# Optimization experiments

Measured on AMD Instinct MI355X. Metric: run time of the kernel, lower is better.

Reference implementation:

```python
import jax, jax.numpy as jnp
import numpy as np

H, DH, M, DIN = 8, 64, 32, 512  # heads, head_dim, cluster_num, input_dim
INNER = H * DH


def setup_inputs() -> dict:
    key = jax.random.key(0)
    ks = jax.random.split(key, 12)
    s = 0.02
    B, N = 4, 16384
    return {
        "x": jax.random.normal(ks[0], (B, N, DIN), jnp.float32),
        "Wx": jax.random.normal(ks[1], (INNER, DIN), jnp.float32) * s,
        "bx": jnp.zeros((INNER,), jnp.float32),
        "Wfx": jax.random.normal(ks[2], (INNER, DIN), jnp.float32) * s,
        "bfx": jnp.zeros((INNER,), jnp.float32),
        "Wslice": jax.random.normal(ks[3], (M, DH), jnp.float32) * s,
        "bslice": jnp.zeros((M,), jnp.float32),
        "Wq": jax.random.normal(ks[4], (DH, DH), jnp.float32) * s,
        "Wk": jax.random.normal(ks[5], (DH, DH), jnp.float32) * s,
        "Wv": jax.random.normal(ks[6], (DH, DH), jnp.float32) * s,
        "Wout": jax.random.normal(ks[7], (DIN, INNER), jnp.float32) * s,
        "bout": jnp.zeros((DIN,), jnp.float32),
        "temperature": jnp.full((1, H, 1, 1), 0.5, jnp.float32),
    }


def reference(x, Wx, bx, Wfx, bfx, Wslice, bslice, Wq, Wk, Wv, Wout, bout, temperature):
    B, N, D = x.shape
    scale = DH ** -0.5
    # projections -> [B, H, N, DH]
    x_mid = (x @ Wx.T + bx).reshape(B, N, H, DH).transpose(0, 2, 1, 3)
    fx_mid = (x @ Wfx.T + bfx).reshape(B, N, H, DH).transpose(0, 2, 1, 3)
    # soft clustering: [B, H, N, M]
    slice_logits = (x_mid @ Wslice.T + bslice) / temperature
    slice_weights = jax.nn.softmax(slice_logits, axis=-1)
    slice_norm = slice_weights.sum(axis=2)  # [B, H, M]
    slice_token = jnp.einsum('bhnd,bhnm->bhmd', fx_mid, slice_weights)
    slice_token = slice_token / (slice_norm[:, :, :, None] + 1e-5)
    # tiny cluster-level attention (M=32)
    q = slice_token @ Wq.T
    k = slice_token @ Wk.T
    v = slice_token @ Wv.T
    attn = jax.nn.softmax(jnp.einsum('bhmd,bhkd->bhmk', q, k) * scale, axis=-1)
    out_slice = jnp.einsum('bhmk,bhkd->bhmd', attn, v)
    # de-slice back to tokens: [B, H, N, DH] -> [B, N, H*DH]
    out_x = jnp.einsum('bhmd,bhnm->bhnd', out_slice, slice_weights)
    out_x = out_x.transpose(0, 2, 1, 3).reshape(B, N, INNER)
    return out_x @ Wout.T + bout
```

## Files before the change

### kernel.cpp

```cpp
#include <hip/hip_runtime.h>

#define B_ 4
#define N_ 16384
#define DIN_ 512
#define H_ 8
#define DH_ 64
#define M_ 32
#define HM_ 256
#define INNER_ 512
#define K2_PARTS 16
#define K2_NIT 32

typedef _Float16 fp16_t;
typedef _Float16 h8 __attribute__((ext_vector_type(8)));
typedef _Float16 h4 __attribute__((ext_vector_type(4)));
typedef float f4 __attribute__((ext_vector_type(4)));


__device__ __forceinline__ int swz(int n, int hm) {
  return ((((hm >> 3) ^ ((n >> 3) & 3)) << 3) | (hm & 7));
}

__global__ __launch_bounds__(256) void k0_prep(
    const float* __restrict__ Wx, const float* __restrict__ bx,
    const float* __restrict__ Wslice, const float* __restrict__ bslice,
    const float* __restrict__ temperature,
    fp16_t* __restrict__ Wcb, float* __restrict__ bcomp) {
  __shared__ float ws[M_ * DH_];
  const int h = blockIdx.x;
  const int tid = threadIdx.x;
  for (int i = tid; i < M_ * DH_; i += 256) ws[i] = Wslice[i];
  __syncthreads();
  const float invt = 1.0f / temperature[h];
  for (int m = 0; m < M_; ++m) {
    const int hm = h * M_ + m;
    for (int k = tid; k < DIN_; k += 256) {
      float acc = 0.f;
      #pragma unroll 16
      for (int d = 0; d < DH_; ++d)
        acc += ws[m * DH_ + d] * Wx[(size_t)(h * DH_ + d) * DIN_ + k];
      const int tile = (k >> 5) * 16 + (hm >> 4);
      const int ln = (((k >> 3) & 3) << 4) + (hm & 15);
      Wcb[(size_t)tile * 512 + ln * 8 + (k & 7)] = (fp16_t)(acc * invt);
    }
  }
  if (tid < M_) {
    const int m = tid;
    float acc = bslice[m];
    for (int d = 0; d < DH_; ++d) acc += ws[m * DH_ + d] * bx[h * DH_ + d];
    bcomp[h * M_ + m] = acc * invt;
  }
}

__global__ __launch_bounds__(256) void k1_logits(
    const float* __restrict__ x, const fp16_t* __restrict__ Wcb,
    const float* __restrict__ bcomp, fp16_t* __restrict__ w_blk,
    fp16_t* __restrict__ wt_blk, fp16_t* __restrict__ xt_blk) {
  __shared__ __align__(16) fp16_t smem[16896];
  fp16_t* lt = smem;
  const int tid = threadIdx.x;
  const int lane = tid & 63;
  const int wv = tid >> 6;
  const int n0 = blockIdx.x * 64;
  const int b = blockIdx.y;
  f4 acc[4][4] = {};
  const float* xb = x + ((size_t)b * N_ + n0) * DIN_;
  const int lrow = lane & 15;
  const int kb = (lane >> 4) * 8;
  const int xr = tid >> 3, xq = tid & 7;
  const int xt_rt = wv >> 1;
  const int xt_nt = wv & 1;
  const int xt_k = xt_rt * 16 + (lane & 15);
  const int xt_nb = xt_nt * 32 + (lane >> 4) * 8;
  const fp16_t* wp = Wcb + (size_t)(wv * 4) * 512 + lane * 8;

  f4 xv[2];
  h8 bfv[4];
  #pragma unroll
  for (int i = 0; i < 2; ++i)
    xv[i] = *(const f4*)(xb + (size_t)(xr + i * 32) * DIN_ + xq * 4);
  #pragma unroll
  for (int t = 0; t < 4; ++t)
    bfv[t] = *(const h8*)(wp + (size_t)t * 512);
  #pragma unroll
  for (int i = 0; i < 2; ++i) {
    h4 hv = {(fp16_t)xv[i].x, (fp16_t)xv[i].y, (fp16_t)xv[i].z, (fp16_t)xv[i].w};
    *(h4*)&smem[(xr + i * 32) * 40 + xq * 4] = hv;
  }
  __syncthreads();

  for (int kt = 0; kt < 16; ++kt) {
    fp16_t* lxc = smem + (kt & 1) * 2560;
    fp16_t* lxn = smem + ((kt & 1) ^ 1) * 2560;
    h8 bf[4];
    #pragma unroll
    for (int t = 0; t < 4; ++t) bf[t] = bfv[t];
    if (kt < 15) {
      const int k0n = (kt + 1) * 32;
      #pragma unroll
      for (int i = 0; i < 2; ++i)
        xv[i] = *(const f4*)(xb + (size_t)(xr + i * 32) * DIN_ + k0n + xq * 4);
      #pragma unroll
      for (int t = 0; t < 4; ++t)
        bfv[t] = *(const h8*)(wp + (size_t)((kt + 1) * 16 + t) * 512);
    }
    {
      h8 tx;
      #pragma unroll
      for (int e = 0; e < 8; ++e) tx[e] = lxc[(xt_nb + e) * 40 + xt_k];
      *(h8*)(xt_blk + (((size_t)(b * 32 + kt * 2 + xt_rt) * (N_ / 32)) + (n0 >> 5) + xt_nt) * 512 + lane * 8) = tx;
    }
    h8 af[4];
    #pragma unroll
    for (int t = 0; t < 4; ++t) af[t] = *(const h8*)&lxc[(t * 16 + lrow) * 40 + kb];
    #pragma unroll
    for (int tn = 0; tn < 4; ++tn)
      #pragma unroll
      for (int tc = 0; tc < 4; ++tc)
        acc[tn][tc] = __builtin_amdgcn_mfma_f32_16x16x32_f16(af[tn], bf[tc], acc[tn][tc], 0, 0, 0);
    if (kt < 15) {
      #pragma unroll
      for (int i = 0; i < 2; ++i) {
        h4 hv = {(fp16_t)xv[i].x, (fp16_t)xv[i].y, (fp16_t)xv[i].z, (fp16_t)xv[i].w};
        *(h4*)&lxn[(xr + i * 32) * 40 + xq * 4] = hv;
      }
    }
    __syncthreads();
  }

  const int col = lane & 15;
  const int rgrp = (lane >> 4) * 4;
  float bc[2][2];
  #pragma unroll
  for (int s = 0; s < 2; ++s) {
    bc[s][0] = bcomp[wv * 64 + s * 32 + col];
    bc[s][1] = bcomp[wv * 64 + s * 32 + 16 + col];
  }
  #pragma unroll
  for (int s = 0; s < 2; ++s) {
    const int hmA = wv * 64 + s * 32 + col;
    #pragma unroll
    for (int tn = 0; tn < 4; ++tn)
      #pragma unroll
      for (int r = 0; r < 4; ++r) {
        const int nl = tn * 16 + rgrp + r;
        lt[nl * 264 + swz(nl, hmA)] = (fp16_t)(acc[tn][2 * s][r] + bc[s][0]);
        lt[nl * 264 + swz(nl, hmA + 16)] = (fp16_t)(acc[tn][2 * s + 1][r] + bc[s][1]);
      }
  }
  __syncthreads();

  #pragma unroll
  for (int p = 0; p < 2; ++p) {
    const int pair = tid + p * 256;
    const int nl = pair >> 3, h = pair & 7;
    const int sw = (nl >> 3) & 3;
    h8 ch[4];
    #pragma unroll
    for (int q = 0; q < 4; ++q)
      ch[q] = *(const h8*)&lt[nl * 264 + ((h * 4 + q) ^ sw) * 8];
    float v[32];
    #pragma unroll
    for (int q = 0; q < 4; ++q)
      #pragma unroll
      for (int e = 0; e < 8; ++e) v[q * 8 + e] = (float)ch[q][e];
    float mx = v[0];
    #pragma unroll
    for (int j = 1; j < 32; ++j) mx = fmaxf(mx, v[j]);
    float sm = 0.f;
    #pragma unroll
    for (int j = 0; j < 32; ++j) { v[j] = __expf(v[j] - mx); sm += v[j]; }
    const float inv = __builtin_amdgcn_rcpf(sm);
    h8 oc[4];
    #pragma unroll
    for (int q = 0; q < 4; ++q)
      #pragma unroll
      for (int e = 0; e < 8; ++e) oc[q][e] = (fp16_t)(v[q * 8 + e] * inv);
    #pragma unroll
    for (int q = 0; q < 4; ++q)
      *(h8*)&lt[nl * 264 + ((h * 4 + q) ^ sw) * 8] = oc[q];
  }
  __syncthreads();

  #pragma unroll
  for (int p = 0; p < 8; ++p) {
    const int tile = p * 4 + wv;
    const int nt_l = tile >> 3, hmb = tile & 7;
    const int n_l = nt_l * 16 + (lane & 15);
    const int g = hmb * 4 + (lane >> 4);
    const int sw = (n_l >> 3) & 3;
    h8 v = *(const h8*)&lt[n_l * 264 + (g ^ sw) * 8];
    *(h8*)(w_blk + (((size_t)(b * (N_ / 16) + (n0 >> 4) + nt_l)) * 8 + hmb) * 512 + lane * 8) = v;
  }

  #pragma unroll
  for (int p = 0; p < 8; ++p) {
    const int tile = p * 4 + wv;
    const int hmt = tile >> 1, ntl = tile & 1;
    const int hm = hmt * 16 + (lane & 15);
    const int nb = ntl * 32 + (lane >> 4) * 8;
    h8 v;
    #pragma unroll
    for (int e = 0; e < 8; ++e) {
      const int n = nb + e;
      v[e] = lt[n * 264 + swz(n, hm)];
    }
    *(h8*)(wt_blk + (((size_t)(b * 16 + hmt)) * (N_ / 32) + (n0 >> 5) + ntl) * 512 + lane * 8) = v;
  }
}

__global__ __launch_bounds__(256) void k2_S(
    const fp16_t* __restrict__ wt_blk, const fp16_t* __restrict__ xt_blk,
    float* __restrict__ P, float* __restrict__ norm) {
  const int tid = threadIdx.x, lane = tid & 63, wv = tid >> 6;
  const int hm0 = (blockIdx.x & 1) * 128;
  const int kc0 = (blockIdx.x >> 1) * 128;
  const int part = blockIdx.y;
  const int nt0 = part * K2_NIT;
  const int b = blockIdx.z;
  const int hmw = (wv & 1) * 64, kw = (wv >> 1) * 64;
  const int hmt0 = (hm0 + hmw) >> 4;
  const int kt0 = (kc0 + kw) >> 4;
  const fp16_t* ap = wt_blk + (((size_t)(b * 16 + hmt0)) * (N_ / 32) + nt0) * 512 + lane * 8;
  const fp16_t* bp = xt_blk + (((size_t)(b * 32 + kt0)) * (N_ / 32) + nt0) * 512 + lane * 8;
  const size_t arow = (size_t)(N_ / 32) * 512;
  f4 acc[4][4] = {};
  float ns[4] = {0.f, 0.f, 0.f, 0.f};
  const bool do_norm = (kc0 == 0) && (kw == 0);

  h8 aA[4], bA[4], aB[4], bB[4];
  #pragma unroll
  for (int t = 0; t < 4; ++t) {
    aA[t] = *(const h8*)(ap + (size_t)t * arow);
    bA[t] = *(const h8*)(bp + (size_t)t * arow);
  }
  for (int it = 0; it < K2_NIT; it += 2) {
    #pragma unroll
    for (int t = 0; t < 4; ++t) {
      aB[t] = *(const h8*)(ap + (size_t)t * arow + (it + 1) * 512);
      bB[t] = *(const h8*)(bp + (size_t)t * arow + (it + 1) * 512);
    }
    #pragma unroll
    for (int tn = 0; tn < 4; ++tn)
      #pragma unroll
      for (int tc = 0; tc < 4; ++tc)
        acc[tn][tc] = __builtin_amdgcn_mfma_f32_16x16x32_f16(aA[tn], bA[tc], acc[tn][tc], 0, 0, 0);
    if (do_norm) {
      #pragma unroll
      for (int t = 0; t < 4; ++t)
        #pragma unroll
        for (int e = 0; e < 8; ++e) ns[t] += (float)aA[t][e];
    }
    if (it + 2 < K2_NIT) {
      #pragma unroll
      for (int t = 0; t < 4; ++t) {
        aA[t] = *(const h8*)(ap + (size_t)t * arow + (it + 2) * 512);
        bA[t] = *(const h8*)(bp + (size_t)t * arow + (it + 2) * 512);
      }
    }
    #pragma unroll
    for (int tn = 0; tn < 4; ++tn)
      #pragma unroll
      for (int tc = 0; tc < 4; ++tc)
        acc[tn][tc] = __builtin_amdgcn_mfma_f32_16x16x32_f16(aB[tn], bB[tc], acc[tn][tc], 0, 0, 0);
    if (do_norm) {
      #pragma unroll
      for (int t = 0; t < 4; ++t)
        #pragma unroll
        for (int e = 0; e < 8; ++e) ns[t] += (float)aB[t][e];
    }
  }

  if (do_norm) {
    #pragma unroll
    for (int t = 0; t < 4; ++t) {
      ns[t] += __shfl_xor(ns[t], 16);
      ns[t] += __shfl_xor(ns[t], 32);
    }
    if (lane < 16) {
      #pragma unroll
      for (int t = 0; t < 4; ++t)
        atomicAdd(&norm[b * HM_ + (hmt0 + t) * 16 + lane], ns[t]);
    }
  }
  float* Pp = P + (((size_t)part * B_ + b) * HM_ + hm0 + hmw) * DIN_ + kc0 + kw;
  const int rg = (lane >> 4) * 4;
  #pragma unroll
  for (int tn = 0; tn < 4; ++tn)
    #pragma unroll
    for (int tc = 0; tc < 4; ++tc)
      #pragma unroll
      for (int r = 0; r < 4; ++r)
        Pp[(size_t)(tn * 16 + rg + r) * DIN_ + tc * 16 + (lane & 15)] = acc[tn][tc][r];
}

__global__ __launch_bounds__(256) void k2r_reduce(
    const float* __restrict__ P, float* __restrict__ S) {
  const size_t idx = (size_t)blockIdx.x * 256 + threadIdx.x;
  const f4* P4 = (const f4*)P;
  f4 a = P4[idx];
  #pragma unroll
  for (int p = 1; p < K2_PARTS; ++p)
    a += P4[(size_t)p * (B_ * HM_ * DIN_ / 4) + idx];
  ((f4*)S)[idx] = a;
}

__global__ __launch_bounds__(256) void k3a_st(
    const float* __restrict__ S, const float* __restrict__ Wfx,
    const float* __restrict__ bfx, const float* __restrict__ norm,
    float* __restrict__ st) {
  const int mq = blockIdx.x;
  const int h = blockIdx.y;
  const int b = blockIdx.z;
  const int tid = threadIdx.x;
  const int m = mq * 4 + (tid >> 6);
  const int d = tid & 63;
  const float* sr = S + ((size_t)b * HM_ + h * M_ + m) * DIN_;
  const float* wr = Wfx + (size_t)(h * DH_ + d) * DIN_;
  float acc = 0.f;
  #pragma unroll 8
  for (int k = 0; k < DIN_; k += 4) {
    f4 a = *(const f4*)(sr + k);
    f4 bb = *(const f4*)(wr + k);
    acc += a.x * bb.x + a.y * bb.y + a.z * bb.z + a.w * bb.w;
  }
  const float nr = norm[b * HM_ + h * M_ + m];
  st[(((size_t)b * H_ + h) * M_ + m) * DH_ + d] =
      (acc + bfx[h * DH_ + d] * nr) / (nr + 1e-5f);
}

__global__ __launch_bounds__(256) void k3b_attn(
    const float* __restrict__ st_g, const float* __restrict__ Wq,
    const float* __restrict__ Wk, const float* __restrict__ Wv,
    float* __restrict__ os_g) {
  __shared__ float st[32][65], qs[32][65], ks[32][65], vs[32][65], at[32][33];
  const int h = blockIdx.x, b = blockIdx.y, tid = threadIdx.x;
  const float* stp = st_g + ((size_t)b * H_ + h) * M_ * DH_;
  for (int i = tid; i < 2048; i += 256) st[i >> 6][i & 63] = stp[i];
  __syncthreads();
  for (int i = tid; i < 2048; i += 256) {
    const int m = i >> 6, d = i & 63;
    float aq = 0, ak = 0, av = 0;
    #pragma unroll 8
    for (int dd = 0; dd < 64; ++dd) {
      const float s = st[m][dd];
      aq += s * Wq[d * 64 + dd];
      ak += s * Wk[d * 64 + dd];
      av += s * Wv[d * 64 + dd];
    }
    qs[m][d] = aq; ks[m][d] = ak; vs[m][d] = av;
  }
  __syncthreads();
  for (int i = tid; i < 1024; i += 256) {
    const int m = i >> 5, j = i & 31;
    float a = 0;
    #pragma unroll 8
    for (int d = 0; d < 64; ++d) a += qs[m][d] * ks[j][d];
    at[m][j] = a * 0.125f;
  }
  __syncthreads();
  if (tid < 32) {
    const int m = tid;
    float mx = -1e30f;
    for (int j = 0; j < 32; ++j) mx = fmaxf(mx, at[m][j]);
    float sm = 0;
    for (int j = 0; j < 32; ++j) { const float e = __expf(at[m][j] - mx); at[m][j] = e; sm += e; }
    const float inv = 1.0f / sm;
    for (int j = 0; j < 32; ++j) at[m][j] *= inv;
  }
  __syncthreads();
  float* osp = os_g + ((size_t)b * H_ + h) * M_ * DH_;
  for (int i = tid; i < 2048; i += 256) {
    const int m = i >> 6, d = i & 63;
    float a = 0;
    #pragma unroll 8
    for (int j = 0; j < 32; ++j) a += at[m][j] * vs[j][d];
    osp[i] = a;
  }
}

__global__ __launch_bounds__(256) void k3c_ct(
    const float* __restrict__ os_g, const float* __restrict__ Wout,
    fp16_t* __restrict__ Ct_blk) {
  const int tid = threadIdx.x, lane = tid & 63, wv = tid >> 6;
  const int b = blockIdx.y;
  const int ti = blockIdx.x * 4 + wv;
  const int kkt = ti >> 3, hmb = ti & 7;
  const int kk = kkt * 16 + (lane & 15);
  h8 outv;
  #pragma unroll
  for (int e = 0; e < 8; ++e) {
    const int hm = hmb * 32 + (lane >> 4) * 8 + e;
    const int h = hm >> 5, m = hm & 31;
    const float* op = os_g + (((size_t)b * H_ + h) * M_ + m) * DH_;
    const float* wp = Wout + (size_t)kk * INNER_ + h * DH_;
    float acc = 0.f;
    #pragma unroll
    for (int d = 0; d < 64; d += 4) {
      f4 a = *(const f4*)(op + d);
      f4 w4 = *(const f4*)(wp + d);
      acc += a.x * w4.x + a.y * w4.y + a.z * w4.z + a.w * w4.w;
    }
    outv[e] = (fp16_t)acc;
  }
  *(h8*)(Ct_blk + (((size_t)(b * 32 + kkt)) * 8 + hmb) * 512 + lane * 8) = outv;
}

__global__ __launch_bounds__(256) void k4_out(
    const fp16_t* __restrict__ w_blk, const fp16_t* __restrict__ Ct_blk,
    const float* __restrict__ bout, float* __restrict__ out) {
  const int tid = threadIdx.x, lane = tid & 63, wv = tid >> 6;
  const int kk0 = blockIdx.x * 128;
  const int n0 = blockIdx.y * 128;
  const int b = blockIdx.z;
  const int nh = (wv & 1) * 64, kh = (wv >> 1) * 64;
  const int nt0 = (n0 + nh) >> 4;
  const int kkt0 = (kk0 + kh) >> 4;
  const fp16_t* ap = w_blk + ((size_t)(b * (N_ / 16) + nt0)) * 8 * 512 + lane * 8;
  const fp16_t* bp = Ct_blk + ((size_t)(b * 32 + kkt0)) * 8 * 512 + lane * 8;
  f4 acc[4][4] = {};

  #pragma unroll
  for (int hmb = 0; hmb < 8; ++hmb) {
    h8 af[4], bf[4];
    #pragma unroll
    for (int t = 0; t < 4; ++t) af[t] = *(const h8*)(ap + (size_t)t * 8 * 512 + hmb * 512);
    #pragma unroll
    for (int t = 0; t < 4; ++t) bf[t] = *(const h8*)(bp + (size_t)t * 8 * 512 + hmb * 512);
    #pragma unroll
    for (int tn = 0; tn < 4; ++tn)
      #pragma unroll
      for (int tc = 0; tc < 4; ++tc)
        acc[tn][tc] = __builtin_amdgcn_mfma_f32_16x16x32_f16(af[tn], bf[tc], acc[tn][tc], 0, 0, 0);
  }
  const int rg = (lane >> 4) * 4;
  #pragma unroll
  for (int tc = 0; tc < 4; ++tc) {
    const int kk = kk0 + kh + tc * 16 + (lane & 15);
    const float bo = bout[kk];
    #pragma unroll
    for (int tn = 0; tn < 4; ++tn)
      #pragma unroll
      for (int r = 0; r < 4; ++r) {
        const int n = n0 + nh + tn * 16 + rg + r;
        out[((size_t)b * N_ + n) * DIN_ + kk] = acc[tn][tc][r] + bo;
      }
  }
}

extern "C" void kernel_launch(void* const* d_in, const int* in_sizes, int n_in,
                              void* d_out, int out_size, void* d_ws, size_t ws_size,
                              hipStream_t stream) {
  (void)in_sizes; (void)n_in; (void)out_size; (void)ws_size;
  const float* x       = (const float*)d_in[0];
  const float* Wx      = (const float*)d_in[1];
  const float* bx      = (const float*)d_in[2];
  const float* Wfx     = (const float*)d_in[3];
  const float* bfx     = (const float*)d_in[4];
  const float* Wslice  = (const float*)d_in[5];
  const float* bslice  = (const float*)d_in[6];
  const float* Wq      = (const float*)d_in[7];
  const float* Wk      = (const float*)d_in[8];
  const float* Wv      = (const float*)d_in[9];
  const float* Wout    = (const float*)d_in[10];
  const float* bout    = (const float*)d_in[11];
  const float* temp    = (const float*)d_in[12];
  float* out = (float*)d_out;

  char* ws = (char*)d_ws;
  fp16_t* w_blk  = (fp16_t*)ws;
  fp16_t* wt_blk = (fp16_t*)(ws + 33554432);
  fp16_t* xt_blk = (fp16_t*)(ws + 67108864);
  float*  S      = (float*)(ws + 134217728);
  float*  norm   = (float*)(ws + 136314880);
  float*  st     = (float*)(ws + 136318976);
  float*  os     = (float*)(ws + 136581120);
  fp16_t* Ct_blk = (fp16_t*)(ws + 136843264);
  fp16_t* Wcb    = (fp16_t*)(ws + 137891840);
  float*  bcomp  = (float*)(ws + 138153984);
  float*  P      = (float*)(ws + 138158080);

  hipMemsetAsync(norm, 0, (size_t)B_ * HM_ * 4, stream);
  k0_prep<<<dim3(H_), 256, 0, stream>>>(Wx, bx, Wslice, bslice, temp, Wcb, bcomp);
  k1_logits<<<dim3(N_ / 64, B_), 256, 0, stream>>>(x, Wcb, bcomp, w_blk, wt_blk, xt_blk);
  k2_S<<<dim3(8, K2_PARTS, B_), 256, 0, stream>>>(wt_blk, xt_blk, P, norm);
  k2r_reduce<<<dim3(B_ * HM_ * DIN_ / 4 / 256), 256, 0, stream>>>(P, S);
  k3a_st<<<dim3(8, H_, B_), 256, 0, stream>>>(S, Wfx, bfx, norm, st);
  k3b_attn<<<dim3(H_, B_), 256, 0, stream>>>(st, Wq, Wk, Wv, os);
  k3c_ct<<<dim3(64, B_), 256, 0, stream>>>(os, Wout, Ct_blk);
  k4_out<<<dim3(DIN_ / 128, N_ / 128, B_), 256, 0, stream>>>(w_blk, Ct_blk, bout, out);
}
```

Baseline: 525.9 us.

## Stage full x tile in swizzled LDS and deepen register prefetch in GEMMs

k1_logits now loads the whole 64x512 x tile into LDS up front, using an XOR-swizzled layout. This removes the per-k-step double buffering and its __syncthreads. k2_S deepens its register prefetch from two to four stages, and k4_out double-buffers its register loads, so more global loads are in flight ahead of the MFMAs. The cost is 64KB of LDS per block in k1 and more registers in k2, which may reduce occupancy.

```diff
diff --git a/kernel.cpp b/kernel.cpp
--- a/kernel.cpp
+++ b/kernel.cpp
@@ -19,6 +19,10 @@
 
 __device__ __forceinline__ int swz(int n, int hm) {
   return ((((hm >> 3) ^ ((n >> 3) & 3)) << 3) | (hm & 7));
+}
+
+__device__ __forceinline__ int xoff(int row, int k) {
+  return row * 512 + ((((k >> 3) ^ (row & 7)) << 3) | (k & 7));
 }
 
 __global__ __launch_bounds__(256) void k0_prep(
@@ -56,7 +60,7 @@
     const float* __restrict__ x, const fp16_t* __restrict__ Wcb,
     const float* __restrict__ bcomp, fp16_t* __restrict__ w_blk,
     fp16_t* __restrict__ wt_blk, fp16_t* __restrict__ xt_blk) {
-  __shared__ __align__(16) fp16_t smem[16896];
+  __shared__ __align__(16) fp16_t smem[64 * 512];
   fp16_t* lt = smem;
   const int tid = threadIdx.x;
   const int lane = tid & 63;
@@ -66,40 +70,31 @@
   f4 acc[4][4] = {};
   const float* xb = x + ((size_t)b * N_ + n0) * DIN_;
   const int lrow = lane & 15;
-  const int kb = (lane >> 4) * 8;
-  const int xr = tid >> 3, xq = tid & 7;
+  const int kgq = lane >> 4;
   const int xt_rt = wv >> 1;
   const int xt_nt = wv & 1;
   const int xt_k = xt_rt * 16 + (lane & 15);
   const int xt_nb = xt_nt * 32 + (lane >> 4) * 8;
   const fp16_t* wp = Wcb + (size_t)(wv * 4) * 512 + lane * 8;
 
-  f4 xv[2];
+  #pragma unroll
+  for (int i = 0; i < 32; ++i) {
+    const int fid = tid + i * 256;
+    const int row = fid >> 7, c4 = fid & 127;
+    f4 v = *(const f4*)(xb + (size_t)row * DIN_ + c4 * 4);
+    h4 hv = {(fp16_t)v.x, (fp16_t)v.y, (fp16_t)v.z, (fp16_t)v.w};
+    *(h4*)&smem[xoff(row, c4 * 4)] = hv;
+  }
   h8 bfv[4];
   #pragma unroll
-  for (int i = 0; i < 2; ++i)
-    xv[i] = *(const f4*)(xb + (size_t)(xr + i * 32) * DIN_ + xq * 4);
-  #pragma unroll
-  for (int t = 0; t < 4; ++t)
-    bfv[t] = *(const h8*)(wp + (size_t)t * 512);
-  #pragma unroll
-  for (int i = 0; i < 2; ++i) {
-    h4 hv = {(fp16_t)xv[i].x, (fp16_t)xv[i].y, (fp16_t)xv[i].z, (fp16_t)xv[i].w};
-    *(h4*)&smem[(xr + i * 32) * 40 + xq * 4] = hv;
-  }
+  for (int t = 0; t < 4; ++t) bfv[t] = *(const h8*)(wp + (size_t)t * 512);
   __syncthreads();
 
   for (int kt = 0; kt < 16; ++kt) {
-    fp16_t* lxc = smem + (kt & 1) * 2560;
-    fp16_t* lxn = smem + ((kt & 1) ^ 1) * 2560;
     h8 bf[4];
     #pragma unroll
     for (int t = 0; t < 4; ++t) bf[t] = bfv[t];
     if (kt < 15) {
-      const int k0n = (kt + 1) * 32;
-      #pragma unroll
-      for (int i = 0; i < 2; ++i)
-        xv[i] = *(const f4*)(xb + (size_t)(xr + i * 32) * DIN_ + k0n + xq * 4);
       #pragma unroll
       for (int t = 0; t < 4; ++t)
         bfv[t] = *(const h8*)(wp + (size_t)((kt + 1) * 16 + t) * 512);
@@ -107,26 +102,21 @@
     {
       h8 tx;
       #pragma unroll
-      for (int e = 0; e < 8; ++e) tx[e] = lxc[(xt_nb + e) * 40 + xt_k];
+      for (int e = 0; e < 8; ++e)
+        tx[e] = smem[xoff(xt_nb + e, kt * 32 + xt_k)];
       *(h8*)(xt_blk + (((size_t)(b * 32 + kt * 2 + xt_rt) * (N_ / 32)) + (n0 >> 5) + xt_nt) * 512 + lane * 8) = tx;
     }
     h8 af[4];
     #pragma unroll
-    for (int t = 0; t < 4; ++t) af[t] = *(const h8*)&lxc[(t * 16 + lrow) * 40 + kb];
+    for (int t = 0; t < 4; ++t)
+      af[t] = *(const h8*)&smem[xoff(t * 16 + lrow, kt * 32 + kgq * 8)];
     #pragma unroll
     for (int tn = 0; tn < 4; ++tn)
       #pragma unroll
       for (int tc = 0; tc < 4; ++tc)
         acc[tn][tc] = __builtin_amdgcn_mfma_f32_16x16x32_f16(af[tn], bf[tc], acc[tn][tc], 0, 0, 0);
-    if (kt < 15) {
-      #pragma unroll
-      for (int i = 0; i < 2; ++i) {
-        h4 hv = {(fp16_t)xv[i].x, (fp16_t)xv[i].y, (fp16_t)xv[i].z, (fp16_t)xv[i].w};
-        *(h4*)&lxn[(xr + i * 32) * 40 + xq * 4] = hv;
-      }
-    }
-    __syncthreads();
-  }
+  }
+  __syncthreads();
 
   const int col = lane & 15;
   const int rgrp = (lane >> 4) * 4;
@@ -208,6 +198,26 @@
     *(h8*)(wt_blk + (((size_t)(b * 16 + hmt)) * (N_ / 32) + (n0 >> 5) + ntl) * 512 + lane * 8) = v;
   }
 }
+
+#define K2_LD(S, IT)                                                        \
+  do {                                                                      \
+    _Pragma("unroll") for (int t = 0; t < 4; ++t) {                         \
+      S##a[t] = *(const h8*)(ap + (size_t)t * arow + (IT) * 512);           \
+      S##b[t] = *(const h8*)(bp + (size_t)t * arow + (IT) * 512);           \
+    }                                                                       \
+  } while (0)
+#define K2_MM(S)                                                            \
+  do {                                                                      \
+    _Pragma("unroll") for (int tn = 0; tn < 4; ++tn)                        \
+      _Pragma("unroll") for (int tc = 0; tc < 4; ++tc)                      \
+        acc[tn][tc] = __builtin_amdgcn_mfma_f32_16x16x32_f16(               \
+            S##a[tn], S##b[tc], acc[tn][tc], 0, 0, 0);                      \
+    if (do_norm) {                                                          \
+      _Pragma("unroll") for (int t = 0; t < 4; ++t)                         \
+        _Pragma("unroll") for (int e = 0; e < 8; ++e)                       \
+          ns[t] += (float)S##a[t][e];                                       \
+    }                                                                       \
+  } while (0)
 
 __global__ __launch_bounds__(256) void k2_S(
     const fp16_t* __restrict__ wt_blk, const fp16_t* __restrict__ xt_blk,
@@ -228,47 +238,13 @@
   float ns[4] = {0.f, 0.f, 0.f, 0.f};
   const bool do_norm = (kc0 == 0) && (kw == 0);
 
-  h8 aA[4], bA[4], aB[4], bB[4];
-  #pragma unroll
-  for (int t = 0; t < 4; ++t) {
-    aA[t] = *(const h8*)(ap + (size_t)t * arow);
-    bA[t] = *(const h8*)(bp + (size_t)t * arow);
-  }
-  for (int it = 0; it < K2_NIT; it += 2) {
-    #pragma unroll
-    for (int t = 0; t < 4; ++t) {
-      aB[t] = *(const h8*)(ap + (size_t)t * arow + (it + 1) * 512);
-      bB[t] = *(const h8*)(bp + (size_t)t * arow + (it + 1) * 512);
-    }
-    #pragma unroll
-    for (int tn = 0; tn < 4; ++tn)
-      #pragma unroll
-      for (int tc = 0; tc < 4; ++tc)
-        acc[tn][tc] = __builtin_amdgcn_mfma_f32_16x16x32_f16(aA[tn], bA[tc], acc[tn][tc], 0, 0, 0);
-    if (do_norm) {
-      #pragma unroll
-      for (int t = 0; t < 4; ++t)
-        #pragma unroll
-        for (int e = 0; e < 8; ++e) ns[t] += (float)aA[t][e];
-    }
-    if (it + 2 < K2_NIT) {
-      #pragma unroll
-      for (int t = 0; t < 4; ++t) {
-        aA[t] = *(const h8*)(ap + (size_t)t * arow + (it + 2) * 512);
-        bA[t] = *(const h8*)(bp + (size_t)t * arow + (it + 2) * 512);
-      }
-    }
-    #pragma unroll
-    for (int tn = 0; tn < 4; ++tn)
-      #pragma unroll
-      for (int tc = 0; tc < 4; ++tc)
-        acc[tn][tc] = __builtin_amdgcn_mfma_f32_16x16x32_f16(aB[tn], bB[tc], acc[tn][tc], 0, 0, 0);
-    if (do_norm) {
-      #pragma unroll
-      for (int t = 0; t < 4; ++t)
-        #pragma unroll
-        for (int e = 0; e < 8; ++e) ns[t] += (float)aB[t][e];
-    }
+  h8 Aa[4], Ab[4], Ba[4], Bb[4], Ca[4], Cb[4], Da[4], Db[4];
+  K2_LD(A, 0); K2_LD(B, 1); K2_LD(C, 2); K2_LD(D, 3);
+  for (int it = 0; it < K2_NIT; it += 4) {
+    K2_MM(A); if (it + 4 < K2_NIT) K2_LD(A, it + 4);
+    K2_MM(B); if (it + 5 < K2_NIT) K2_LD(B, it + 5);
+    K2_MM(C); if (it + 6 < K2_NIT) K2_LD(C, it + 6);
+    K2_MM(D); if (it + 7 < K2_NIT) K2_LD(D, it + 7);
   }
 
   if (do_norm) {
@@ -406,6 +382,21 @@
   *(h8*)(Ct_blk + (((size_t)(b * 32 + kkt)) * 8 + hmb) * 512 + lane * 8) = outv;
 }
 
+#define K4_LD(S, HMB)                                                       \
+  do {                                                                      \
+    _Pragma("unroll") for (int t = 0; t < 4; ++t) {                         \
+      S##a[t] = *(const h8*)(ap + (size_t)t * 8 * 512 + (HMB) * 512);       \
+      S##b[t] = *(const h8*)(bp + (size_t)t * 8 * 512 + (HMB) * 512);       \
+    }                                                                       \
+  } while (0)
+#define K4_MM(S)                                                            \
+  do {                                                                      \
+    _Pragma("unroll") for (int tn = 0; tn < 4; ++tn)                        \
+      _Pragma("unroll") for (int tc = 0; tc < 4; ++tc)                      \
+        acc[tn][tc] = __builtin_amdgcn_mfma_f32_16x16x32_f16(               \
+            S##a[tn], S##b[tc], acc[tn][tc], 0, 0, 0);                      \
+  } while (0)
+
 __global__ __launch_bounds__(256) void k4_out(
     const fp16_t* __restrict__ w_blk, const fp16_t* __restrict__ Ct_blk,
     const float* __restrict__ bout, float* __restrict__ out) {
@@ -420,18 +411,12 @@
   const fp16_t* bp = Ct_blk + ((size_t)(b * 32 + kkt0)) * 8 * 512 + lane * 8;
   f4 acc[4][4] = {};
 
-  #pragma unroll
-  for (int hmb = 0; hmb < 8; ++hmb) {
-    h8 af[4], bf[4];
-    #pragma unroll
-    for (int t = 0; t < 4; ++t) af[t] = *(const h8*)(ap + (size_t)t * 8 * 512 + hmb * 512);
-    #pragma unroll
-    for (int t = 0; t < 4; ++t) bf[t] = *(const h8*)(bp + (size_t)t * 8 * 512 + hmb * 512);
-    #pragma unroll
-    for (int tn = 0; tn < 4; ++tn)
-      #pragma unroll
-      for (int tc = 0; tc < 4; ++tc)
-        acc[tn][tc] = __builtin_amdgcn_mfma_f32_16x16x32_f16(af[tn], bf[tc], acc[tn][tc], 0, 0, 0);
+  h8 Aa[4], Ab[4], Ba[4], Bb[4];
+  K4_LD(A, 0); K4_LD(B, 1);
+  #pragma unroll
+  for (int hmb = 0; hmb < 8; hmb += 2) {
+    K4_MM(A); if (hmb + 2 < 8) K4_LD(A, hmb + 2);
+    K4_MM(B); if (hmb + 3 < 8) K4_LD(B, hmb + 3);
   }
   const int rg = (lane >> 4) * 4;
   #pragma unroll
```

Measured after the change: 535.4 us. About the same (+1.8%).

## Stage full x tile in LDS once and split k1 across eight waves

Applied to the files above, without the earlier changes.

k1_logits now loads the whole 64x512 x tile into a swizzled 64 KB LDS buffer up front, instead of double-buffering 32-column slices with a barrier at each k step. The block grows to 512 threads, and each wave computes 32 cluster columns instead of 64. Per-iteration barriers are gone and the accumulator register footprint is halved. The cost is much higher LDS use per block, which can lower occupancy, and the global loads are no longer overlapped with the MFMA loop.

```diff
diff --git a/kernel.cpp b/kernel.cpp
--- a/kernel.cpp
+++ b/kernel.cpp
@@ -19,6 +19,10 @@
 
 __device__ __forceinline__ int swz(int n, int hm) {
   return ((((hm >> 3) ^ ((n >> 3) & 3)) << 3) | (hm & 7));
+}
+
+__device__ __forceinline__ int xoff(int row, int k) {
+  return row * 512 + ((((k >> 3) ^ (row & 7)) << 3) | (k & 7));
 }
 
 __global__ __launch_bounds__(256) void k0_prep(
@@ -52,108 +56,85 @@
   }
 }
 
-__global__ __launch_bounds__(256) void k1_logits(
+__global__ __launch_bounds__(512) void k1_logits(
     const float* __restrict__ x, const fp16_t* __restrict__ Wcb,
     const float* __restrict__ bcomp, fp16_t* __restrict__ w_blk,
     fp16_t* __restrict__ wt_blk, fp16_t* __restrict__ xt_blk) {
-  __shared__ __align__(16) fp16_t smem[16896];
+  __shared__ __align__(16) fp16_t smem[64 * 512];
   fp16_t* lt = smem;
   const int tid = threadIdx.x;
   const int lane = tid & 63;
   const int wv = tid >> 6;
   const int n0 = blockIdx.x * 64;
   const int b = blockIdx.y;
-  f4 acc[4][4] = {};
+  f4 acc[4][2] = {};
   const float* xb = x + ((size_t)b * N_ + n0) * DIN_;
   const int lrow = lane & 15;
-  const int kb = (lane >> 4) * 8;
-  const int xr = tid >> 3, xq = tid & 7;
+  const int kgq = lane >> 4;
   const int xt_rt = wv >> 1;
   const int xt_nt = wv & 1;
   const int xt_k = xt_rt * 16 + (lane & 15);
   const int xt_nb = xt_nt * 32 + (lane >> 4) * 8;
-  const fp16_t* wp = Wcb + (size_t)(wv * 4) * 512 + lane * 8;
-
-  f4 xv[2];
-  h8 bfv[4];
-  #pragma unroll
-  for (int i = 0; i < 2; ++i)
-    xv[i] = *(const f4*)(xb + (size_t)(xr + i * 32) * DIN_ + xq * 4);
-  #pragma unroll
-  for (int t = 0; t < 4; ++t)
-    bfv[t] = *(const h8*)(wp + (size_t)t * 512);
-  #pragma unroll
-  for (int i = 0; i < 2; ++i) {
-    h4 hv = {(fp16_t)xv[i].x, (fp16_t)xv[i].y, (fp16_t)xv[i].z, (fp16_t)xv[i].w};
-    *(h4*)&smem[(xr + i * 32) * 40 + xq * 4] = hv;
-  }
+  const fp16_t* wp = Wcb + (size_t)(wv * 2) * 512 + lane * 8;
+
+  #pragma unroll
+  for (int i = 0; i < 16; ++i) {
+    const int fid = tid + i * 512;
+    const int row = fid >> 7, c4 = fid & 127;
+    f4 v = *(const f4*)(xb + (size_t)row * DIN_ + c4 * 4);
+    h4 hv = {(fp16_t)v.x, (fp16_t)v.y, (fp16_t)v.z, (fp16_t)v.w};
+    *(h4*)&smem[xoff(row, c4 * 4)] = hv;
+  }
+  h8 bfv[2];
+  #pragma unroll
+  for (int t = 0; t < 2; ++t) bfv[t] = *(const h8*)(wp + (size_t)t * 512);
   __syncthreads();
 
   for (int kt = 0; kt < 16; ++kt) {
-    fp16_t* lxc = smem + (kt & 1) * 2560;
-    fp16_t* lxn = smem + ((kt & 1) ^ 1) * 2560;
-    h8 bf[4];
-    #pragma unroll
-    for (int t = 0; t < 4; ++t) bf[t] = bfv[t];
+    h8 bf[2];
+    #pragma unroll
+    for (int t = 0; t < 2; ++t) bf[t] = bfv[t];
     if (kt < 15) {
-      const int k0n = (kt + 1) * 32;
-      #pragma unroll
-      for (int i = 0; i < 2; ++i)
-        xv[i] = *(const f4*)(xb + (size_t)(xr + i * 32) * DIN_ + k0n + xq * 4);
-      #pragma unroll
-      for (int t = 0; t < 4; ++t)
+      #pragma unroll
+      for (int t = 0; t < 2; ++t)
         bfv[t] = *(const h8*)(wp + (size_t)((kt + 1) * 16 + t) * 512);
     }
-    {
+    if (wv < 4) {
       h8 tx;
       #pragma unroll
-      for (int e = 0; e < 8; ++e) tx[e] = lxc[(xt_nb + e) * 40 + xt_k];
+      for (int e = 0; e < 8; ++e)
+        tx[e] = smem[xoff(xt_nb + e, kt * 32 + xt_k)];
       *(h8*)(xt_blk + (((size_t)(b * 32 + kt * 2 + xt_rt) * (N_ / 32)) + (n0 >> 5) + xt_nt) * 512 + lane * 8) = tx;
     }
     h8 af[4];
     #pragma unroll
-    for (int t = 0; t < 4; ++t) af[t] = *(const h8*)&lxc[(t * 16 + lrow) * 40 + kb];
+    for (int t = 0; t < 4; ++t)
+      af[t] = *(const h8*)&smem[xoff(t * 16 + lrow, kt * 32 + kgq * 8)];
     #pragma unroll
     for (int tn = 0; tn < 4; ++tn)
       #pragma unroll
-      for (int tc = 0; tc < 4; ++tc)
+      for (int tc = 0; tc < 2; ++tc)
         acc[tn][tc] = __builtin_amdgcn_mfma_f32_16x16x32_f16(af[tn], bf[tc], acc[tn][tc], 0, 0, 0);
-    if (kt < 15) {
-      #pragma unroll
-      for (int i = 0; i < 2; ++i) {
-        h4 hv = {(fp16_t)xv[i].x, (fp16_t)xv[i].y, (fp16_t)xv[i].z, (fp16_t)xv[i].w};
-        *(h4*)&lxn[(xr + i * 32) * 40 + xq * 4] = hv;
-      }
-    }
-    __syncthreads();
-  }
+  }
+  __syncthreads();
 
   const int col = lane & 15;
   const int rgrp = (lane >> 4) * 4;
-  float bc[2][2];
-  #pragma unroll
-  for (int s = 0; s < 2; ++s) {
-    bc[s][0] = bcomp[wv * 64 + s * 32 + col];
-    bc[s][1] = bcomp[wv * 64 + s * 32 + 16 + col];
-  }
-  #pragma unroll
-  for (int s = 0; s < 2; ++s) {
-    const int hmA = wv * 64 + s * 32 + col;
-    #pragma unroll
-    for (int tn = 0; tn < 4; ++tn)
-      #pragma unroll
-      for (int r = 0; r < 4; ++r) {
-        const int nl = tn * 16 + rgrp + r;
-        lt[nl * 264 + swz(nl, hmA)] = (fp16_t)(acc[tn][2 * s][r] + bc[s][0]);
-        lt[nl * 264 + swz(nl, hmA + 16)] = (fp16_t)(acc[tn][2 * s + 1][r] + bc[s][1]);
-      }
-  }
-  __syncthreads();
-
-  #pragma unroll
-  for (int p = 0; p < 2; ++p) {
-    const int pair = tid + p * 256;
-    const int nl = pair >> 3, h = pair & 7;
+  const float bc0 = bcomp[wv * 32 + col];
+  const float bc1 = bcomp[wv * 32 + 16 + col];
+  const int hmA = wv * 32 + col;
+  #pragma unroll
+  for (int tn = 0; tn < 4; ++tn)
+    #pragma unroll
+    for (int r = 0; r < 4; ++r) {
+      const int nl = tn * 16 + rgrp + r;
+      lt[nl * 264 + swz(nl, hmA)] = (fp16_t)(acc[tn][0][r] + bc0);
+      lt[nl * 264 + swz(nl, hmA + 16)] = (fp16_t)(acc[tn][1][r] + bc1);
+    }
+  __syncthreads();
+
+  {
+    const int nl = tid >> 3, h = tid & 7;
     const int sw = (nl >> 3) & 3;
     h8 ch[4];
     #pragma unroll
@@ -183,8 +164,8 @@
   __syncthreads();
 
   #pragma unroll
-  for (int p = 0; p < 8; ++p) {
-    const int tile = p * 4 + wv;
+  for (int p = 0; p < 4; ++p) {
+    const int tile = p * 8 + wv;
     const int nt_l = tile >> 3, hmb = tile & 7;
     const int n_l = nt_l * 16 + (lane & 15);
     const int g = hmb * 4 + (lane >> 4);
@@ -194,8 +175,8 @@
   }
 
   #pragma unroll
-  for (int p = 0; p < 8; ++p) {
-    const int tile = p * 4 + wv;
+  for (int p = 0; p < 4; ++p) {
+    const int tile = p * 8 + wv;
     const int hmt = tile >> 1, ntl = tile & 1;
     const int hm = hmt * 16 + (lane & 15);
     const int nb = ntl * 32 + (lane >> 4) * 8;
@@ -482,7 +463,7 @@
 
   hipMemsetAsync(norm, 0, (size_t)B_ * HM_ * 4, stream);
   k0_prep<<<dim3(H_), 256, 0, stream>>>(Wx, bx, Wslice, bslice, temp, Wcb, bcomp);
-  k1_logits<<<dim3(N_ / 64, B_), 256, 0, stream>>>(x, Wcb, bcomp, w_blk, wt_blk, xt_blk);
+  k1_logits<<<dim3(N_ / 64, B_), 512, 0, stream>>>(x, Wcb, bcomp, w_blk, wt_blk, xt_blk);
   k2_S<<<dim3(8, K2_PARTS, B_), 256, 0, stream>>>(wt_blk, xt_blk, P, norm);
   k2r_reduce<<<dim3(B_ * HM_ * DIN_ / 4 / 256), 256, 0, stream>>>(P, S);
   k3a_st<<<dim3(8, H_, B_), 256, 0, stream>>>(S, Wfx, bfx, norm, st);
```

New measurement: 523.9 us. Within noise of the previous version (-0.4%).
